# Kernel tuning notes

Measured on AMD Instinct MI355X. Metric: run time of the kernel, lower is better.

The kernel has to match this reference:

```python
import jax, jax.numpy as jnp
import numpy as np

DIM = 512
HEADS = 8
DIM_HEAD = 64
ROT_DIM = DIM_HEAD // 2  # RotaryEmbedding(dim_head // 2)
B = 4
N = 8192


def rotate_every_two(x):
    # '... (d j) -> ... d j', j=2 ; (x1, x2) -> (-x2, x1) interleaved back
    x1 = x[..., 0::2]
    x2 = x[..., 1::2]
    return jnp.stack((-x2, x1), axis=-1).reshape(x.shape)


def apply_rotary_emb(freqs, t):
    # freqs: [1,1,n,rot_dim]; rotary on first rot_dim channels, passthrough rest
    rot_dim = freqs.shape[-1]
    t_rot, t_pass = t[..., :rot_dim], t[..., rot_dim:]
    t_rot = t_rot * jnp.cos(freqs) + rotate_every_two(t_rot) * jnp.sin(freqs)
    return jnp.concatenate((t_rot, t_pass), axis=-1)


def rotary_freqs(n):
    # lucidrains RotaryEmbedding(ROT_DIM): inv_freq over ROT_DIM//2, repeated r=2
    inv_freq = 1.0 / (10000.0 ** (jnp.arange(0, ROT_DIM, 2, dtype=jnp.float32) / ROT_DIM))
    f = jnp.arange(n, dtype=jnp.float32)[:, None] * inv_freq[None, :]  # [n, ROT_DIM//2]
    return jnp.repeat(f, 2, axis=-1)  # [n, ROT_DIM]


def setup_inputs() -> dict:
    key = jax.random.key(0)
    ks = jax.random.split(key, 8)
    inner = HEADS * DIM_HEAD
    s = lambda fan_in: 1.0 / np.sqrt(fan_in)
    return {
        "x": jax.random.normal(ks[0], (B, N, DIM), dtype=jnp.float32),
        "w_qkv": jax.random.uniform(ks[1], (DIM, inner * 3), jnp.float32, -s(DIM), s(DIM)),
        "w_q_logits": jax.random.uniform(ks[2], (DIM_HEAD, 1), jnp.float32, -s(DIM_HEAD), s(DIM_HEAD)),
        "w_k_logits": jax.random.uniform(ks[3], (DIM_HEAD // 2, 1), jnp.float32, -s(DIM_HEAD // 2), s(DIM_HEAD // 2)),
        "w_r": jax.random.uniform(ks[4], (DIM_HEAD // 2, DIM_HEAD), jnp.float32, -s(DIM_HEAD // 2), s(DIM_HEAD // 2)),
        "b_r": jax.random.uniform(ks[5], (DIM_HEAD,), jnp.float32, -s(DIM_HEAD // 2), s(DIM_HEAD // 2)),
        "w_out": jax.random.uniform(ks[6], (inner, DIM), jnp.float32, -s(inner), s(inner)),
        "b_out": jax.random.uniform(ks[7], (DIM,), jnp.float32, -s(inner), s(inner)),
    }


def reference(x, w_qkv, w_q_logits, w_k_logits, w_r, b_r, w_out, b_out):
    b, n, _ = x.shape
    h, d = HEADS, DIM_HEAD
    scale = d ** -0.5

    qkv = x @ w_qkv  # [b,n,3*h*d]
    q, k, v = jnp.split(qkv, 3, axis=-1)
    to_bhnd = lambda t: t.reshape(b, n, h, d).transpose(0, 2, 1, 3)
    q, k, v = to_bhnd(q), to_bhnd(k), to_bhnd(v)

    freqs = rotary_freqs(n)[None, None]  # [1,1,n,ROT_DIM]
    q_aggr = apply_rotary_emb(freqs, q)
    k_aggr = apply_rotary_emb(freqs, k)
    v_aggr = v

    q_attn = jax.nn.softmax((q @ w_q_logits)[..., 0] * scale, axis=-1)  # [b,h,n]
    global_q = jnp.einsum('bhn,bhnd->bhd', q_attn, q_aggr)[:, :, None]  # [b,h,1,d]

    kk = (k * global_q).reshape(b, h, n, d // 2, 2).sum(-1)  # sum adjacent pairs -> [b,h,n,d/2]
    k_attn = jax.nn.softmax((kk @ w_k_logits)[..., 0] * scale, axis=-1)
    global_k = jnp.einsum('bhn,bhnd->bhd', k_attn, k_aggr)[:, :, None]  # [b,h,1,d]

    u = (v_aggr * global_k).reshape(b, h, n, d // 2, 2).sum(-1)  # [b,h,n,d/2]
    r = u @ w_r + b_r  # [b,h,n,d]
    r = r + q
    r = r.transpose(0, 2, 1, 3).reshape(b, n, h * d)
    return r @ w_out + b_out
```

## Files before the change

kernel.cpp:

```cpp
#include <hip/hip_runtime.h>
#include <hip/hip_bf16.h>

typedef __attribute__((ext_vector_type(8))) short s16x8;
typedef __attribute__((ext_vector_type(4))) short s16x4;
typedef __attribute__((ext_vector_type(4))) float f32x4;

#define SEQ 8192

__device__ __forceinline__ float bf2f(short s){
  union { unsigned u; float f; } c; c.u = ((unsigned)(unsigned short)s) << 16; return c.f;
}
__device__ __forceinline__ short f2bf(float f){
  __hip_bfloat16 h = __float2bfloat16(f);
  short s; __builtin_memcpy(&s, &h, 2); return s;
}

__global__ __launch_bounds__(256) void build_tab_pk(unsigned* __restrict__ tab){
  int idx = blockIdx.x*256 + threadIdx.x;
  int n = idx >> 6, d = idx & 63;
  float c, s;
  if (d < 32){
    float ex = -(float)(d & ~1) / 32.0f;
    float invf = __expf(ex * 9.210340371976184f);
    float f = (float)n * invf;
    c = cosf(f);
    s = sinf(f);
    s = (d & 1) ? s : -s;
  } else { c = 1.f; s = 0.f; }
  unsigned lo = (unsigned)(unsigned short)f2bf(c);
  unsigned hi = (unsigned)(unsigned short)f2bf(s);
  tab[idx] = lo | (hi << 16);
}

__global__ __launch_bounds__(256) void cvt_x(const float* __restrict__ in, __hip_bfloat16* __restrict__ out){
  int i = blockIdx.x*256 + threadIdx.x;
  float4 v = reinterpret_cast<const float4*>(in)[i];
  s16x4 o = { f2bf(v.x), f2bf(v.y), f2bf(v.z), f2bf(v.w) };
  reinterpret_cast<s16x4*>(out)[i] = o;
}

__global__ __launch_bounds__(256) void transpose_cvt(const float* __restrict__ in, __hip_bfloat16* __restrict__ out,
                                                     int R, int C){
  __shared__ float tile[32][33];
  int c0 = blockIdx.x*32, r0 = blockIdx.y*32;
  int tx = threadIdx.x & 31, ty = threadIdx.x >> 5;
  #pragma unroll
  for (int i = ty; i < 32; i += 8) tile[i][tx] = in[(size_t)(r0+i)*C + c0 + tx];
  __syncthreads();
  #pragma unroll
  for (int i = ty; i < 32; i += 8) out[(size_t)(c0+i)*R + r0 + tx] = __float2bfloat16(tile[tx][i]);
}

#define SCHED0() __builtin_amdgcn_sched_barrier(0)
#define BAR()    __builtin_amdgcn_s_barrier()

template<int MODE>
__global__ __launch_bounds__(512, 2) void gemm256(
    const __hip_bfloat16* __restrict__ A, const __hip_bfloat16* __restrict__ BT,
    int M, int Nn, int K,
    __hip_bfloat16* __restrict__ oQ, __hip_bfloat16* __restrict__ oK, __hip_bfloat16* __restrict__ oV,
    float* __restrict__ oF, const float* __restrict__ bias)
{
  constexpr int NBUF  = (MODE == 0) ? 4 : 3;
  constexpr int AHEAD = (MODE == 0) ? 3 : 2;
  constexpr int BUFSZ = (MODE == 0) ? 32768 : 24576;
  constexpr int NSTG  = (MODE == 0) ? 4 : 3;
  constexpr int BN    = (MODE == 0) ? 256 : 128;
  constexpr int MI    = (MODE == 0) ? 8 : 4;
  __shared__ __align__(16) char lds[NBUF * BUFSZ];

  const int t = threadIdx.x;
  const int lane = t & 63, wid = t >> 6;
  const int lr = lane & 15, lg = lane >> 4;
  const int wm   = (MODE == 0) ? (wid >> 2) * 128 : (wid >> 1) * 64;
  const int wn64 = (MODE == 0) ? (wid & 3) * 64   : (wid & 1) * 64;

  int nwg = gridDim.x, per = nwg >> 3, wg = blockIdx.x;
  int swz = (wg & 7) * per + (wg >> 3);
  int nblk = Nn / BN;
  int bm = (swz / nblk) << 8;
  int bn = (swz % nblk) * BN;

  const int NKT = K >> 5;

  const __hip_bfloat16* spp[NSTG];
  int dofs[NSTG];
  #pragma unroll
  for (int i = 0; i < NSTG; ++i){
    int g = (i < 2) ? (t + i*512) : ((MODE == 0) ? (t + (i-2)*512) : t);
    int row = g >> 2, ch = g & 3;
    int sch = ch ^ ((row & 3) ^ ((row >> 2) & 3));
    spp[i] = (i < 2 ? A + (size_t)(bm + row)*K : BT + (size_t)(bn + row)*K) + sch*8;
    dofs[i] = ((i < 2) ? 0 : 16384) + g*16;
  }
  #define STG(i, kt, bufbase) __builtin_amdgcn_global_load_lds( \
      (const __attribute__((address_space(1))) void*)(spp[i] + (size_t)(kt)*32), \
      (__attribute__((address_space(3))) void*)(lds + (bufbase) + dofs[i]), 16, 0, 0)

  #pragma unroll
  for (int tl = 0; tl < AHEAD; ++tl)
    #pragma unroll
    for (int i = 0; i < NSTG; ++i) STG(i, tl, tl*BUFSZ);

  f32x4 acc[MI][4] = {};
  #define SWB(r) ((((r) & 3) ^ (((r) >> 2) & 3)) << 4)
  #define RD_A(h) _Pragma("unroll") for (int f = 0; f < 4; ++f){ \
      int r = wm + (h)*64 + f*16 + lr; \
      af[f] = *reinterpret_cast<const s16x8*>(lb + (r << 6) + ((lg << 4) ^ SWB(r))); }
  #define RD_B() _Pragma("unroll") for (int f = 0; f < 4; ++f){ \
      int r = wn64 + f*16 + lr; \
      bfr[f] = *reinterpret_cast<const s16x8*>(lb + 16384 + (r << 6) + ((lg << 4) ^ SWB(r))); }
  #define MFMA16(h) do { __builtin_amdgcn_s_setprio(1); \
    _Pragma("unroll") for (int m2 = 0; m2 < 4; ++m2) \
    _Pragma("unroll") for (int ni = 0; ni < 4; ++ni) \
      acc[(h)*4+m2][ni] = __builtin_amdgcn_mfma_f32_16x16x32_bf16(bfr[ni], af[m2], acc[(h)*4+m2][ni], 0, 0, 0); \
    __builtin_amdgcn_s_setprio(0); } while(0)

  int rIdx = 0, sIdx = AHEAD % NBUF;
  for (int kt = 0; kt < NKT; ++kt){
    if (MODE == 0){
      if (kt + 2 < NKT)       asm volatile("s_waitcnt vmcnt(8)" ::: "memory");
      else if (kt + 2 == NKT) asm volatile("s_waitcnt vmcnt(4)" ::: "memory");
      else                    asm volatile("s_waitcnt vmcnt(0)" ::: "memory");
    } else {
      if (kt + 1 < NKT)       asm volatile("s_waitcnt vmcnt(3)" ::: "memory");
      else                    asm volatile("s_waitcnt vmcnt(0)" ::: "memory");
    }
    SCHED0(); BAR(); SCHED0();
    const char* lb = lds + rIdx*BUFSZ;
    const int sb = sIdx*BUFSZ;
    const bool stg = (kt + AHEAD) < NKT;
    s16x8 af[4], bfr[4];
    RD_A(0); RD_B();
    if (stg){ STG(0, kt+AHEAD, sb); STG(1, kt+AHEAD, sb); }
    if (MODE == 1 && stg){ STG(2, kt+AHEAD, sb); }
    BAR(); SCHED0();
    MFMA16(0);
    if (MODE == 0){
      BAR(); SCHED0();
      RD_A(1);
      if (stg){ STG(2, kt+AHEAD, sb); STG(3, kt+AHEAD, sb); }
      BAR(); SCHED0();
      MFMA16(1);
    }
    rIdx = (rIdx + 1 == NBUF) ? 0 : rIdx + 1;
    sIdx = (sIdx + 1 == NBUF) ? 0 : sIdx + 1;
  }
  BAR();

  if (MODE == 0){
    char* reg = lds + wid*16384;
    #pragma unroll
    for (int mi = 0; mi < 8; ++mi){
      #pragma unroll
      for (int ni = 0; ni < 4; ++ni){
        int tok = mi*16 + lr;
        int sl = (ni*4 + lg) ^ (tok & 15);
        ushort4 w4;
        w4.x = (unsigned short)f2bf(acc[mi][ni][0]);
        w4.y = (unsigned short)f2bf(acc[mi][ni][1]);
        w4.z = (unsigned short)f2bf(acc[mi][ni][2]);
        w4.w = (unsigned short)f2bf(acc[mi][ni][3]);
        *reinterpret_cast<unsigned long long*>(reg + tok*128 + sl*8) =
            *reinterpret_cast<unsigned long long*>(&w4);
      }
    }
    asm volatile("s_waitcnt lgkmcnt(0)" ::: "memory");
    SCHED0();
    int gcol = bn + wn64;
    int ts = gcol >> 9, rem = gcol & 511, h = rem >> 6;
    __hip_bfloat16* dstT = (ts == 0) ? oQ : ((ts == 1) ? oK : oV);
    int tokbase = bm + wm;
    int bb = tokbase >> 13;
    dstT += ((size_t)(bb*8 + h)) << 19;
    #pragma unroll
    for (int p2 = 0; p2 < 16; ++p2){
      int tok = p2*8 + (lane >> 3);
      int l0 = (lane & 7) * 2;
      unsigned long long u0 = *reinterpret_cast<const unsigned long long*>(reg + tok*128 + ((l0 ^ (tok & 15)))*8);
      unsigned long long u1 = *reinterpret_cast<const unsigned long long*>(reg + tok*128 + (((l0+1) ^ (tok & 15)))*8);
      int n = (tokbase + tok) & 8191;
      unsigned long long o2[2] = { u0, u1 };
      *reinterpret_cast<s16x8*>(dstT + ((size_t)n << 6) + (lane & 7)*8) =
          *reinterpret_cast<const s16x8*>(o2);
    }
  } else {
    #pragma unroll
    for (int mi = 0; mi < MI; ++mi){
      #pragma unroll
      for (int ni = 0; ni < 4; ++ni){
        int gc = bn + wn64 + ni*16 + lg*4;
        int gr = bm + wm + mi*16 + lr;
        float4 bv = *reinterpret_cast<const float4*>(bias + gc);
        float4 o;
        o.x = acc[mi][ni][0] + bv.x;
        o.y = acc[mi][ni][1] + bv.y;
        o.z = acc[mi][ni][2] + bv.z;
        o.w = acc[mi][ni][3] + bv.w;
        *reinterpret_cast<float4*>(oF + (size_t)gr*Nn + gc) = o;
      }
    }
  }
  #undef STG
  #undef SWB
  #undef RD_A
  #undef RD_B
  #undef MFMA16
}

__global__ __launch_bounds__(256) void fused_stats(
    const __hip_bfloat16* __restrict__ T, const float* __restrict__ svec, int svstride, float scale,
    const unsigned* __restrict__ tab, float* __restrict__ outp)
{
  int chunk = blockIdx.x, bh = blockIdx.y;
  int t = threadIdx.x, lane = t & 63, w = t >> 6;
  __shared__ float sv[64];
  __shared__ float ev[256];
  __shared__ float redv[4][64];
  __shared__ float rede[4];
  if (t < 64) sv[t] = svec[svstride*bh + t] * scale;
  __syncthreads();

  int n = chunk*256 + t;
  const __hip_bfloat16* row = T + ((size_t)bh*SEQ + n)*64;
  float s = 0.f;
  #pragma unroll
  for (int dv = 0; dv < 8; ++dv){
    s16x8 v8 = *reinterpret_cast<const s16x8*>(row + dv*8);
    #pragma unroll
    for (int e = 0; e < 8; ++e) s += bf2f(v8[e]) * sv[dv*8 + e];
  }
  ev[t] = __expf(s);
  __syncthreads();

  const short* Tsh = reinterpret_cast<const short*>(T + ((size_t)bh*SEQ)*64);
  float acc = 0.f, se = 0.f;
  int nb = chunk*256 + w*64;
  #pragma unroll 4
  for (int i = 0; i < 64; ++i){
    int n2 = nb + i;
    float e = ev[w*64 + i];
    float xv = bf2f(Tsh[(size_t)n2*64 + lane]);
    float xo = __shfl_xor(xv, 1, 64);
    unsigned cs = tab[n2*64 + lane];
    float c  = bf2f((short)(cs & 0xffff));
    float s2 = bf2f((short)(cs >> 16));
    acc += e * (xv*c + xo*s2);
    se += e;
  }
  redv[w][lane] = acc;
  if (lane == 0) rede[w] = se;
  __syncthreads();
  if (t < 64){
    float* ob = outp + (size_t)(bh*32 + chunk)*66;
    ob[2 + t] = redv[0][t] + redv[1][t] + redv[2][t] + redv[3][t];
    if (t == 0) ob[1] = rede[0] + rede[1] + rede[2] + rede[3];
  }
}

__global__ void final_combine(const float* __restrict__ parts, float* __restrict__ gvec,
                              const float* __restrict__ wkl, float* __restrict__ gqwk)
{
  int bh = blockIdx.x, d = threadIdx.x;
  const float* pp = parts + (size_t)bh*32*66;
  float tot = 0.f, g = 0.f;
  #pragma unroll 4
  for (int i = 0; i < 32; ++i){ tot += pp[i*66 + 1]; g += pp[i*66 + 2 + d]; }
  g /= tot;
  gvec[bh*64 + d] = g;
  if (gqwk) gqwk[bh*64 + d] = g * wkl[d >> 1] * 0.125f;
}

__global__ __launch_bounds__(256) void epilogue_r(
    const __hip_bfloat16* __restrict__ vT, const __hip_bfloat16* __restrict__ qT,
    const float* __restrict__ gk, const float* __restrict__ wr, const float* __restrict__ br,
    __hip_bfloat16* __restrict__ rb)
{
  int idx = blockIdx.x*256 + threadIdx.x;
  int bh = idx >> 13, nl = idx & 8191;
  int b = bh >> 3, h = bh & 7;
  const __hip_bfloat16* vrow = vT + (size_t)idx*64;
  const __hip_bfloat16* qrow = qT + (size_t)idx*64;
  const float* gkb = gk + bh*64;
  float u[32];
  #pragma unroll
  for (int dv = 0; dv < 8; ++dv){
    s16x8 v8 = *reinterpret_cast<const s16x8*>(vrow + dv*8);
    #pragma unroll
    for (int e = 0; e < 8; e += 2){
      int d = dv*8 + e;
      u[d >> 1] = bf2f(v8[e])*gkb[d] + bf2f(v8[e+1])*gkb[d+1];
    }
  }
  __hip_bfloat16* rrow = rb + ((size_t)(b*SEQ + nl))*512 + h*64;
  #pragma unroll 2
  for (int dv = 0; dv < 8; ++dv){
    s16x8 q8 = *reinterpret_cast<const s16x8*>(qrow + dv*8);
    s16x8 o8;
    #pragma unroll
    for (int e = 0; e < 8; ++e){
      int d = dv*8 + e;
      float a2 = br[d] + bf2f(q8[e]);
      #pragma unroll
      for (int j = 0; j < 32; ++j) a2 += u[j] * wr[j*64 + d];
      o8[e] = f2bf(a2);
    }
    *reinterpret_cast<s16x8*>(rrow + dv*8) = o8;
  }
}

extern "C" void kernel_launch(void* const* d_in, const int* in_sizes, int n_in,
                              void* d_out, int out_size, void* d_ws, size_t ws_size,
                              hipStream_t stream)
{
  (void)in_sizes; (void)n_in; (void)out_size; (void)ws_size;
  const float* x    = (const float*)d_in[0];
  const float* wqkv = (const float*)d_in[1];
  const float* wql  = (const float*)d_in[2];
  const float* wkl  = (const float*)d_in[3];
  const float* wr   = (const float*)d_in[4];
  const float* br   = (const float*)d_in[5];
  const float* wout = (const float*)d_in[6];
  const float* bout = (const float*)d_in[7];
  float* out = (float*)d_out;

  char* p = (char*)d_ws;
  auto alloc = [&](size_t bytes){ char* r = p; p += (bytes + 255) & ~(size_t)255; return r; };
  __hip_bfloat16* xb    = (__hip_bfloat16*)alloc(33554432);
  __hip_bfloat16* wqkvT = (__hip_bfloat16*)alloc(1572864);
  __hip_bfloat16* woutT = (__hip_bfloat16*)alloc(524288);
  __hip_bfloat16* qT = (__hip_bfloat16*)alloc(33554432);
  __hip_bfloat16* kT = (__hip_bfloat16*)alloc(33554432);
  __hip_bfloat16* vT = (__hip_bfloat16*)alloc(33554432);
  __hip_bfloat16* rb = (__hip_bfloat16*)alloc(33554432);
  unsigned* tab = (unsigned*)alloc(2097152);
  float* gq     = (float*)alloc(8192);
  float* gqwk   = (float*)alloc(8192);
  float* gk     = (float*)alloc(8192);

  float* partsQ = (float*)xb;
  float* partsK = partsQ + 32*32*66;

  build_tab_pk<<<2048, 256, 0, stream>>>(tab);
  cvt_x<<<16384, 256, 0, stream>>>(x, xb);
  transpose_cvt<<<dim3(48,16), 256, 0, stream>>>(wqkv, wqkvT, 512, 1536);
  transpose_cvt<<<dim3(16,16), 256, 0, stream>>>(wout, woutT, 512, 512);

  gemm256<0><<<768, 512, 0, stream>>>(xb, wqkvT, 32768, 1536, 512,
                                      qT, kT, vT, nullptr, nullptr);

  fused_stats<<<dim3(32,32), 256, 0, stream>>>(qT, wql, 0, 0.125f, tab, partsQ);
  final_combine<<<32, 64, 0, stream>>>(partsQ, gq, wkl, gqwk);
  fused_stats<<<dim3(32,32), 256, 0, stream>>>(kT, gqwk, 64, 1.0f, tab, partsK);
  final_combine<<<32, 64, 0, stream>>>(partsK, gk, nullptr, nullptr);

  epilogue_r<<<1024, 256, 0, stream>>>(vT, qT, gk, wr, br, rb);

  gemm256<1><<<512, 512, 0, stream>>>(rb, woutT, 32768, 512, 512,
                                      nullptr, nullptr, nullptr, out, bout);
}
```

Measured before the change: 218.6 us.

## Load GEMM B fragments directly from global into registers, stage only A in LDS

```diff
diff --git a/kernel.cpp b/kernel.cpp
--- a/kernel.cpp
+++ b/kernel.cpp
@@ -51,9 +51,6 @@
   for (int i = ty; i < 32; i += 8) out[(size_t)(c0+i)*R + r0 + tx] = __float2bfloat16(tile[tx][i]);
 }
 
-#define SCHED0() __builtin_amdgcn_sched_barrier(0)
-#define BAR()    __builtin_amdgcn_s_barrier()
-
 template<int MODE>
 __global__ __launch_bounds__(512, 2) void gemm256(
     const __hip_bfloat16* __restrict__ A, const __hip_bfloat16* __restrict__ BT,
@@ -61,92 +58,76 @@
     __hip_bfloat16* __restrict__ oQ, __hip_bfloat16* __restrict__ oK, __hip_bfloat16* __restrict__ oV,
     float* __restrict__ oF, const float* __restrict__ bias)
 {
-  constexpr int NBUF  = (MODE == 0) ? 4 : 3;
-  constexpr int AHEAD = (MODE == 0) ? 3 : 2;
-  constexpr int BUFSZ = (MODE == 0) ? 32768 : 24576;
-  constexpr int NSTG  = (MODE == 0) ? 4 : 3;
-  constexpr int BN    = (MODE == 0) ? 256 : 128;
-  constexpr int MI    = (MODE == 0) ? 8 : 4;
-  __shared__ __align__(16) char lds[NBUF * BUFSZ];
-
+  __shared__ __align__(16) char lds[131072];
   const int t = threadIdx.x;
   const int lane = t & 63, wid = t >> 6;
   const int lr = lane & 15, lg = lane >> 4;
-  const int wm   = (MODE == 0) ? (wid >> 2) * 128 : (wid >> 1) * 64;
-  const int wn64 = (MODE == 0) ? (wid & 3) * 64   : (wid & 1) * 64;
+  const int wm   = (wid >> 2) * 128;
+  const int wn64 = (wid & 3) * 64;
 
   int nwg = gridDim.x, per = nwg >> 3, wg = blockIdx.x;
   int swz = (wg & 7) * per + (wg >> 3);
-  int nblk = Nn / BN;
+  int nblk = Nn >> 8;
   int bm = (swz / nblk) << 8;
-  int bn = (swz % nblk) * BN;
+  int bn = (swz % nblk) << 8;
 
   const int NKT = K >> 5;
 
-  const __hip_bfloat16* spp[NSTG];
-  int dofs[NSTG];
-  #pragma unroll
-  for (int i = 0; i < NSTG; ++i){
-    int g = (i < 2) ? (t + i*512) : ((MODE == 0) ? (t + (i-2)*512) : t);
+  const __hip_bfloat16* spp[2];
+  int dofs[2];
+  #pragma unroll
+  for (int i = 0; i < 2; ++i){
+    int g = t + i*512;
     int row = g >> 2, ch = g & 3;
-    int sch = ch ^ ((row & 3) ^ ((row >> 2) & 3));
-    spp[i] = (i < 2 ? A + (size_t)(bm + row)*K : BT + (size_t)(bn + row)*K) + sch*8;
-    dofs[i] = ((i < 2) ? 0 : 16384) + g*16;
-  }
-  #define STG(i, kt, bufbase) __builtin_amdgcn_global_load_lds( \
-      (const __attribute__((address_space(1))) void*)(spp[i] + (size_t)(kt)*32), \
-      (__attribute__((address_space(3))) void*)(lds + (bufbase) + dofs[i]), 16, 0, 0)
-
-  #pragma unroll
-  for (int tl = 0; tl < AHEAD; ++tl)
-    #pragma unroll
-    for (int i = 0; i < NSTG; ++i) STG(i, tl, tl*BUFSZ);
-
-  f32x4 acc[MI][4] = {};
-  #define SWB(r) ((((r) & 3) ^ (((r) >> 2) & 3)) << 4)
-  #define RD_A(h) _Pragma("unroll") for (int f = 0; f < 4; ++f){ \
-      int r = wm + (h)*64 + f*16 + lr; \
-      af[f] = *reinterpret_cast<const s16x8*>(lb + (r << 6) + ((lg << 4) ^ SWB(r))); }
-  #define RD_B() _Pragma("unroll") for (int f = 0; f < 4; ++f){ \
-      int r = wn64 + f*16 + lr; \
-      bfr[f] = *reinterpret_cast<const s16x8*>(lb + 16384 + (r << 6) + ((lg << 4) ^ SWB(r))); }
-  #define MFMA16(h) do { __builtin_amdgcn_s_setprio(1); \
-    _Pragma("unroll") for (int m2 = 0; m2 < 4; ++m2) \
+    int sch = ch ^ ((row & 2) | ((row >> 2) & 1));
+    spp[i] = A + (size_t)(bm + row)*K + sch*8;
+    dofs[i] = g * 16;
+  }
+  #define STG(i, kt3) __builtin_amdgcn_global_load_lds( \
+      (const __attribute__((address_space(1))) void*)(spp[i] + (size_t)(kt3)*32), \
+      (__attribute__((address_space(3))) void*)(lds + (((kt3) & 3) << 14) + dofs[i]), 16, 0, 0)
+
+  const __hip_bfloat16* Bbase = BT + (size_t)(bn + wn64)*K;
+
+  STG(0, 0); STG(1, 0);
+  STG(0, 1); STG(1, 1);
+  STG(0, 2); STG(1, 2);
+  s16x8 bA[4], bB[4];
+  #pragma unroll
+  for (int f = 0; f < 4; ++f)
+    bA[f] = *reinterpret_cast<const s16x8*>(Bbase + (size_t)(f*16 + lr)*K + lg*8);
+
+  f32x4 acc[8][4] = {};
+  s16x8 af[8];
+  #define SWB(r) ((((r) & 2) | (((r) >> 2) & 1)) << 4)
+
+  #define TILE(kt, BU, BNX) do { \
+    if ((kt) == 0)            asm volatile("s_waitcnt vmcnt(8)"  ::: "memory"); \
+    else if ((kt) == 1)       asm volatile("s_waitcnt vmcnt(12)" ::: "memory"); \
+    else if ((kt) < NKT - 2)  asm volatile("s_waitcnt vmcnt(16)" ::: "memory"); \
+    else                      asm volatile("s_waitcnt vmcnt(0)"  ::: "memory"); \
+    __builtin_amdgcn_s_barrier(); \
+    __builtin_amdgcn_sched_barrier(0); \
+    { const char* lb = lds + (((kt) & 3) << 14); \
+      _Pragma("unroll") for (int f = 0; f < 8; ++f){ \
+        int r = wm + f*16 + lr; \
+        af[f] = *reinterpret_cast<const s16x8*>(lb + (r << 6) + ((lg << 4) ^ SWB(r))); } } \
+    if ((kt) + 3 < NKT){ STG(0, (kt)+3); STG(1, (kt)+3); } \
+    if ((kt) + 1 < NKT){ \
+      _Pragma("unroll") for (int f = 0; f < 4; ++f) \
+        BNX[f] = *reinterpret_cast<const s16x8*>(Bbase + (size_t)(f*16 + lr)*K + ((kt)+1)*32 + lg*8); } \
+    __builtin_amdgcn_s_setprio(1); \
+    _Pragma("unroll") for (int mi = 0; mi < 8; ++mi) \
     _Pragma("unroll") for (int ni = 0; ni < 4; ++ni) \
-      acc[(h)*4+m2][ni] = __builtin_amdgcn_mfma_f32_16x16x32_bf16(bfr[ni], af[m2], acc[(h)*4+m2][ni], 0, 0, 0); \
-    __builtin_amdgcn_s_setprio(0); } while(0)
-
-  int rIdx = 0, sIdx = AHEAD % NBUF;
-  for (int kt = 0; kt < NKT; ++kt){
-    if (MODE == 0){
-      if (kt + 2 < NKT)       asm volatile("s_waitcnt vmcnt(8)" ::: "memory");
-      else if (kt + 2 == NKT) asm volatile("s_waitcnt vmcnt(4)" ::: "memory");
-      else                    asm volatile("s_waitcnt vmcnt(0)" ::: "memory");
-    } else {
-      if (kt + 1 < NKT)       asm volatile("s_waitcnt vmcnt(3)" ::: "memory");
-      else                    asm volatile("s_waitcnt vmcnt(0)" ::: "memory");
-    }
-    SCHED0(); BAR(); SCHED0();
-    const char* lb = lds + rIdx*BUFSZ;
-    const int sb = sIdx*BUFSZ;
-    const bool stg = (kt + AHEAD) < NKT;
-    s16x8 af[4], bfr[4];
-    RD_A(0); RD_B();
-    if (stg){ STG(0, kt+AHEAD, sb); STG(1, kt+AHEAD, sb); }
-    if (MODE == 1 && stg){ STG(2, kt+AHEAD, sb); }
-    BAR(); SCHED0();
-    MFMA16(0);
-    if (MODE == 0){
-      BAR(); SCHED0();
-      RD_A(1);
-      if (stg){ STG(2, kt+AHEAD, sb); STG(3, kt+AHEAD, sb); }
-      BAR(); SCHED0();
-      MFMA16(1);
-    }
-    rIdx = (rIdx + 1 == NBUF) ? 0 : rIdx + 1;
-    sIdx = (sIdx + 1 == NBUF) ? 0 : sIdx + 1;
-  }
-  BAR();
+      acc[mi][ni] = __builtin_amdgcn_mfma_f32_16x16x32_bf16(BU[ni], af[mi], acc[mi][ni], 0, 0, 0); \
+    __builtin_amdgcn_s_setprio(0); \
+  } while(0)
+
+  for (int kt = 0; kt < NKT; kt += 2){
+    TILE(kt,     bA, bB);
+    TILE(kt + 1, bB, bA);
+  }
+  __builtin_amdgcn_s_barrier();
 
   if (MODE == 0){
     char* reg = lds + wid*16384;
@@ -166,7 +147,7 @@
       }
     }
     asm volatile("s_waitcnt lgkmcnt(0)" ::: "memory");
-    SCHED0();
+    __builtin_amdgcn_sched_barrier(0);
     int gcol = bn + wn64;
     int ts = gcol >> 9, rem = gcol & 511, h = rem >> 6;
     __hip_bfloat16* dstT = (ts == 0) ? oQ : ((ts == 1) ? oK : oV);
@@ -186,7 +167,7 @@
     }
   } else {
     #pragma unroll
-    for (int mi = 0; mi < MI; ++mi){
+    for (int mi = 0; mi < 8; ++mi){
       #pragma unroll
       for (int ni = 0; ni < 4; ++ni){
         int gc = bn + wn64 + ni*16 + lg*4;
@@ -203,9 +184,7 @@
   }
   #undef STG
   #undef SWB
-  #undef RD_A
-  #undef RD_B
-  #undef MFMA16
+  #undef TILE
 }
 
 __global__ __launch_bounds__(256) void fused_stats(
@@ -356,6 +335,6 @@
 
   epilogue_r<<<1024, 256, 0, stream>>>(vT, qT, gk, wr, br, rb);
 
-  gemm256<1><<<512, 512, 0, stream>>>(rb, woutT, 32768, 512, 512,
+  gemm256<1><<<256, 512, 0, stream>>>(rb, woutT, 32768, 512, 512,
                                       nullptr, nullptr, nullptr, out, bout);
 }
```

Result: slower. 232.0 us (+6.1%).
